# Kernel optimization log

Measured on AMD Instinct MI355X. Metric: run time of the kernel, lower is better.

## Reference

```python
import jax, jax.numpy as jnp
import numpy as np

B, T, M, F, N, H = 2, 1024, 1024, 1024, 16, 64
NEG = -1e30


def _relative_shift(x):
    # x: [b, n, q_len, k_len] -> Transformer-XL pad/reshape shift
    b, h, q_len, k_len = x.shape
    x = jnp.pad(x, ((0, 0), (0, 0), (0, 0), (1, 0)))
    x = x.reshape(b, h, k_len + 1, q_len)[:, :, 1:, :]
    return x.reshape(b, h, q_len, k_len)


def setup_inputs() -> dict:
    key = jax.random.key(0)
    ks = jax.random.split(key, 10)
    std = 0.02
    x = jax.random.normal(ks[0], (B, T, F), jnp.float32)
    rel = jax.random.normal(ks[1], (M + T, F), jnp.float32)
    memory = jax.random.normal(ks[2], (B, M, F), jnp.float32)
    episode_idx = jnp.sort(jax.random.randint(ks[3], (B, M), 0, 4), axis=-1).astype(jnp.int32)
    dones = jax.random.randint(ks[4], (B, T), 0, 2).astype(jnp.int32)
    Wq = jax.random.normal(ks[5], (F, N, H), jnp.float32) * std
    Wk = jax.random.normal(ks[6], (F, N, H), jnp.float32) * std
    Wv = jax.random.normal(ks[7], (F, N, H), jnp.float32) * std
    Wr = jax.random.normal(ks[8], (F, N, H), jnp.float32) * std
    u = jnp.zeros((N, H), jnp.float32)  # bias_init = zeros
    v = jnp.zeros((N, H), jnp.float32)
    Wout = jax.random.normal(ks[9], (N * H, F), jnp.float32) * std
    b_out = jnp.zeros((F,), jnp.float32)
    return {"x": x, "relative_positional_embeddings": rel, "memory": memory,
            "episode_idx": episode_idx, "dones": dones,
            "Wq": Wq, "Wk": Wk, "Wv": Wv, "Wr": Wr, "u": u, "v": v,
            "Wout": Wout, "b_out": b_out}


def reference(x, relative_positional_embeddings, memory, episode_idx, dones,
              Wq, Wk, Wv, Wr, u, v, Wout, b_out):
    scale = 1.0 / np.sqrt(H).astype(np.float32)
    # projections (no bias)
    q = jnp.einsum('btf,fnh->btnh', x, Wq)                      # [B,T,N,H]
    kv_in = jnp.concatenate([memory, x], axis=1)                # [B,M+T,F]
    k = jnp.einsum('bsf,fnh->bsnh', kv_in, Wk)                  # [B,M+T,N,H]
    val = jnp.einsum('bsf,fnh->bsnh', kv_in, Wv)                # [B,M+T,N,H]
    r = jnp.einsum('mf,fnh->mnh', relative_positional_embeddings, Wr)  # [M+T,N,H]

    q_u = q + u[None, None]
    q_v = q + v[None, None]

    # relative positional bias with TXL shift: [B,N,T,M+T]
    bd = jnp.einsum('btnh,mnh->bntm', q_v, r)
    bd = _relative_shift(bd)[..., -(M + T):]
    bias = bd * scale                                           # float32

    # episode mask + causal mask
    qi = episode_idx[:, -1:] + jnp.cumsum(dones, axis=1)        # [B,T]
    ki = jnp.concatenate([episode_idx, qi], axis=1)             # [B,M+T]
    ep_mask = qi[:, None, :, None] == ki[:, None, None, :]      # [B,1,T,M+T]
    causal = jnp.tril(jnp.ones((M + T, M + T), jnp.bool_))[-T:, :][None, None]
    mask = ep_mask & causal                                     # [B,1,T,M+T]

    # attention (matches jax.nn.dot_product_attention XLA path in bf16)
    logits = jnp.einsum('btnh,bsnh->bnts', q_u.astype(jnp.bfloat16), k.astype(jnp.bfloat16))
    logits = logits.astype(jnp.float32) * scale + bias          # [B,N,T,M+T]
    logits = jnp.where(mask, logits, NEG)
    probs = jax.nn.softmax(logits, axis=-1).astype(jnp.bfloat16)
    attn = jnp.einsum('bnts,bsnh->btnh', probs, val.astype(jnp.bfloat16))
    attn = attn.reshape(B, T, N * H).astype(jnp.float32)

    return attn @ Wout + b_out
```

## Files before the change

### kernel.cpp

```cpp
#include <hip/hip_runtime.h>
#include <cstdint>
#include <cstddef>

#define NB 2
#define TT 1024
#define MMEM 1024
#define SS 2048
#define FF 1024
#define NHD 16
#define HD 64

typedef __attribute__((ext_vector_type(8))) short bf16x8;
typedef __attribute__((ext_vector_type(4))) float f32x4;

__device__ __forceinline__ float bf2f(short s){
  unsigned u = ((unsigned)(unsigned short)s) << 16;
  float f; __builtin_memcpy(&f, &u, 4); return f;
}
__device__ __forceinline__ short f2bf(float f){
  unsigned u; __builtin_memcpy(&u, &f, 4);
  u += 0x7fffu + ((u >> 16) & 1u);
  return (short)(u >> 16);
}

typedef const __attribute__((address_space(1))) void gv_t;
typedef __attribute__((address_space(3))) void lv_t;
__device__ __forceinline__ void stage16(const void* g, void* l){
  __builtin_amdgcn_global_load_lds((gv_t*)g, (lv_t*)l, 16, 0, 0);
}

typedef __attribute__((address_space(3))) const short ls3_t;
__device__ __forceinline__ unsigned lds_off(const short* p){
  return (unsigned)(size_t)(ls3_t*)p;
}

template<int OFF>
__device__ __forceinline__ bf16x8 ds_read16(unsigned a){
  bf16x8 d;
  if constexpr (OFF == 0)
    asm volatile("ds_read_b128 %0, %1" : "=v"(d) : "v"(a));
  else
    asm volatile("ds_read_b128 %0, %1 offset:2048" : "=v"(d) : "v"(a));
  return d;
}


__global__ void build_inputs(const float* __restrict__ mem, const float* __restrict__ x,
                             const float* __restrict__ rel,
                             short* __restrict__ kv, short* __restrict__ relo){
  int i = blockIdx.x * blockDim.x + threadIdx.x;
  const int nkv = NB * SS * FF / 4;
  const float* src; short* dst;
  if (i < nkv){
    int idx = i * 4;
    int row = idx >> 10, col = idx & 1023;
    int b = row >> 11, s = row & 2047;
    src = (s < MMEM) ? (mem + ((size_t)b*MMEM + s)*FF + col)
                     : (x   + ((size_t)b*TT + (s - MMEM))*FF + col);
    dst = kv + (size_t)i * 4;
  } else {
    int j = i - nkv;
    if (j >= SS * FF / 4) return;
    src = rel + (size_t)j * 4;
    dst = relo + (size_t)j * 4;
  }
  float4 v = *(const float4*)src;
  short4 o; o.x = f2bf(v.x); o.y = f2bf(v.y); o.z = f2bf(v.z); o.w = f2bf(v.w);
  *(short4*)dst = o;
}

__global__ void transpose_cast5(const float* __restrict__ i0, const float* __restrict__ i1,
                                const float* __restrict__ i2, const float* __restrict__ i3,
                                const float* __restrict__ i4,
                                short* __restrict__ o0, short* __restrict__ o1,
                                short* __restrict__ o2, short* __restrict__ o3,
                                short* __restrict__ o4){
  const float* in; short* out;
  switch (blockIdx.z){
    case 0: in = i0; out = o0; break;
    case 1: in = i1; out = o1; break;
    case 2: in = i2; out = o2; break;
    case 3: in = i3; out = o3; break;
    default: in = i4; out = o4; break;
  }
  __shared__ float tile[32][33];
  int bx = blockIdx.x * 32, by = blockIdx.y * 32;
  int tx = threadIdx.x, ty = threadIdx.y;
  for (int j = ty; j < 32; j += 8)
    tile[j][tx] = in[(size_t)(by + j)*1024 + bx + tx];
  __syncthreads();
  for (int j = ty; j < 32; j += 8)
    out[(size_t)(bx + j)*1024 + by + tx] = f2bf(tile[tx][j]);
}

__global__ void scan_kernel(const int* __restrict__ episode_idx, const int* __restrict__ dones,
                            int* __restrict__ ki, int2* __restrict__ ranges){
  __shared__ int kis[SS];
  __shared__ int wsum[16];
  const int b = blockIdx.x, t = threadIdx.x;
  const int lane = t & 63, wv = t >> 6;
  int v = dones[b*TT + t];
  kis[t] = episode_idx[b*MMEM + t];
  #pragma unroll
  for (int off = 1; off < 64; off <<= 1){
    int tmp = __shfl_up(v, off, 64);
    if (lane >= off) v += tmp;
  }
  if (lane == 63) wsum[wv] = v;
  __syncthreads();
  int add = 0;
  for (int w = 0; w < wv; w++) add += wsum[w];
  v += add;
  const int base = kis[MMEM - 1];
  const int q = base + v;
  kis[MMEM + t] = q;
  ki[b*SS + t] = kis[t];
  ki[b*SS + MMEM + t] = q;
  __syncthreads();
  if (t < 64){
    const int qlo = kis[MMEM + t*16];
    const int qhi = kis[MMEM + t*16 + 15];
    int lo = 0, hi = SS;
    while (lo < hi){ int mid = (lo + hi) >> 1; if (kis[mid] < qlo) lo = mid + 1; else hi = mid; }
    const int s_lo = lo;
    lo = 0; hi = SS;
    const int tgt = qhi + 1;
    while (lo < hi){ int mid = (lo + hi) >> 1; if (kis[mid] < tgt) lo = mid + 1; else hi = mid; }
    int s_hi = lo;
    const int cap = t*16 + 15 + MMEM + 1;
    if (s_hi > cap) s_hi = cap;
    ranges[(b << 6) + t] = make_int2(s_lo, s_hi);
  }
}

__global__ void bias_tables(const short* __restrict__ kbf, const short* __restrict__ rbf,
                            const float* __restrict__ u, const float* __restrict__ v,
                            float* __restrict__ uk, float* __restrict__ vr){
  int i = blockIdx.x * blockDim.x + threadIdx.x;
  const short* p; const float* w; float* outp;
  if (i < NB * NHD * SS){
    int s = i & 2047, n = (i >> 11) & 15, b = i >> 15;
    p = kbf + (size_t)(b * SS + s) * 1024 + n * 64;
    w = u + n * 64;
    outp = uk + (size_t)(b * NHD + n) * SS + s;
  } else {
    int j = i - NB * NHD * SS;
    if (j >= NHD * SS) return;
    int jj = j & 2047, n = j >> 11;
    p = rbf + (size_t)jj * 1024 + n * 64;
    w = v + n * 64;
    outp = vr + (size_t)n * SS + jj;
  }
  float acc = 0.f;
  #pragma unroll
  for (int c = 0; c < 8; c++){
    bf16x8 kv8 = *(const bf16x8*)(p + c * 8);
    float4 w0 = *(const float4*)(w + c * 8);
    float4 w1 = *(const float4*)(w + c * 8 + 4);
    acc += bf2f(kv8[0])*w0.x + bf2f(kv8[1])*w0.y + bf2f(kv8[2])*w0.z + bf2f(kv8[3])*w0.w
         + bf2f(kv8[4])*w1.x + bf2f(kv8[5])*w1.y + bf2f(kv8[6])*w1.z + bf2f(kv8[7])*w1.w;
  }
  *outp = acc;
}

__device__ __forceinline__ void gemm_core_64x64(const short* __restrict__ A,
                                                const short* __restrict__ BT,
                                                int row0, int col0,
                                                short* As, short* Bs,
                                                f32x4 (&acc)[2][2]){
  const int tid = threadIdx.x;
  const int lane = tid & 63, wv = tid >> 6;
  const int lcol = lane & 15, quad = lane >> 4;
  const int wr = (wv >> 1) * 32, wc = (wv & 1) * 32;
  const int sw = lcol & 7;
  const int ch0 = (quad ^ sw) * 8;
  const int ch1 = ((4 + quad) ^ sw) * 8;

  #pragma unroll
  for (int r = 0; r < 2; r++)
    #pragma unroll
    for (int c = 0; c < 2; c++) acc[r][c] = (f32x4){0.f, 0.f, 0.f, 0.f};

  const int rs = tid >> 3, ps = tid & 7;
  const int ls = ps ^ (rs & 7);
  const short* gA = A  + (size_t)(row0 + rs) * 1024 + ls * 8;
  const short* gB = BT + (size_t)(col0 + rs) * 1024 + ls * 8;

  auto STAGE = [&](int k0, int bi){
    short* a = As + bi * 4096 + wv * 512;
    short* b = Bs + bi * 4096 + wv * 512;
    stage16(gA + k0,         a);
    stage16(gA + 32768 + k0, a + 2048);
    stage16(gB + k0,         b);
    stage16(gB + 32768 + k0, b + 2048);
  };

  const unsigned oa0 = lds_off(As) + (unsigned)(((wr + lcol) * 64 + ch0) * 2);
  const unsigned oa1 = lds_off(As) + (unsigned)(((wr + lcol) * 64 + ch1) * 2);
  const unsigned ob0 = lds_off(Bs) + (unsigned)(((wc + lcol) * 64 + ch0) * 2);
  const unsigned ob1 = lds_off(Bs) + (unsigned)(((wc + lcol) * 64 + ch1) * 2);

  STAGE(0, 0);
  STAGE(64, 1);

  #pragma unroll 1
  for (int i = 0; i < 16; ++i){
    const int cur = i - (i / 3) * 3;
    if (i <= 13){
      const int nb = (i + 2) - ((i + 2) / 3) * 3;
      STAGE((i + 2) << 6, nb);
      asm volatile("s_waitcnt vmcnt(8)" ::: "memory");
    } else if (i == 14){
      asm volatile("s_waitcnt vmcnt(4)" ::: "memory");
    } else {
      asm volatile("s_waitcnt vmcnt(0)" ::: "memory");
    }
    __builtin_amdgcn_s_barrier();
    __builtin_amdgcn_sched_barrier(0);
    const unsigned bo = (unsigned)(cur * 8192);
    bf16x8 b00 = ds_read16<0>(ob0 + bo);
    bf16x8 b01 = ds_read16<0>(ob1 + bo);
    bf16x8 b10 = ds_read16<2048>(ob0 + bo);
    bf16x8 b11 = ds_read16<2048>(ob1 + bo);
    bf16x8 a00 = ds_read16<0>(oa0 + bo);
    bf16x8 a01 = ds_read16<0>(oa1 + bo);
    bf16x8 a10 = ds_read16<2048>(oa0 + bo);
    bf16x8 a11 = ds_read16<2048>(oa1 + bo);
    asm volatile("s_waitcnt lgkmcnt(0)" ::: "memory");
    __builtin_amdgcn_sched_barrier(0);
    acc[0][0] = __builtin_amdgcn_mfma_f32_16x16x32_bf16(a00, b00, acc[0][0], 0, 0, 0);
    acc[0][0] = __builtin_amdgcn_mfma_f32_16x16x32_bf16(a01, b01, acc[0][0], 0, 0, 0);
    acc[0][1] = __builtin_amdgcn_mfma_f32_16x16x32_bf16(a00, b10, acc[0][1], 0, 0, 0);
    acc[0][1] = __builtin_amdgcn_mfma_f32_16x16x32_bf16(a01, b11, acc[0][1], 0, 0, 0);
    acc[1][0] = __builtin_amdgcn_mfma_f32_16x16x32_bf16(a10, b00, acc[1][0], 0, 0, 0);
    acc[1][0] = __builtin_amdgcn_mfma_f32_16x16x32_bf16(a11, b01, acc[1][0], 0, 0, 0);
    acc[1][1] = __builtin_amdgcn_mfma_f32_16x16x32_bf16(a10, b10, acc[1][1], 0, 0, 0);
    acc[1][1] = __builtin_amdgcn_mfma_f32_16x16x32_bf16(a11, b11, acc[1][1], 0, 0, 0);
    __builtin_amdgcn_sched_barrier(0);
    __builtin_amdgcn_s_barrier();
  }
}

__global__ __launch_bounds__(256) void proj_gemm(
    const short* __restrict__ kv, const short* __restrict__ relb,
    const short* __restrict__ WkT, const short* __restrict__ WvT,
    const short* __restrict__ WqT, const short* __restrict__ WrT,
    short* __restrict__ kbf, short* __restrict__ vT,
    short* __restrict__ qb, short* __restrict__ rbf,
    const int2* __restrict__ ranges){
  const int z = blockIdx.z;
  const int bx = blockIdx.x;
  const int tid = threadIdx.x;
  const short* A; const short* BT;
  int row0 = bx * 64, qbb = 0;
  __shared__ int s_jm;
  if (z == 0 || z == 1){
    const int bb = row0 >> 11;
    const int srow = row0 & 2047;
    if (srow + 64 <= ranges[bb << 6].x) return;
    A = kv; BT = (z == 0) ? WkT : WvT;
  }
  else if (z == 2){
    if (bx >= 32) return;
    qbb = bx >> 4;
    A = kv + (size_t)(qbb * SS + MMEM) * 1024;
    row0 = (bx & 15) * 64;
    BT = WqT;
  }
  else {
    if (bx >= 32) return;
    if (tid == 0) s_jm = 0x7fffffff;
    __syncthreads();
    if (tid < 128){
      int2 e = ranges[tid];
      int jr = (e.x & ~63) - ((tid & 63) << 4) + 1008;
      atomicMin(&s_jm, jr);
    }
    __syncthreads();
    if (row0 + 64 <= s_jm) return;
    A = relb; BT = WrT;
  }
  const int col0 = blockIdx.y * 64;

  __shared__ __align__(16) short As[3 * 64 * 64];
  __shared__ __align__(16) short Bs[3 * 64 * 64];
  f32x4 acc[2][2];
  gemm_core_64x64(A, BT, row0, col0, As, Bs, acc);

  const int lane = threadIdx.x & 63, wv = threadIdx.x >> 6;
  const int lcol = lane & 15, quad = lane >> 4;
  const int wr = (wv >> 1) * 32, wc = (wv & 1) * 32;
  #pragma unroll
  for (int c = 0; c < 2; c++){
    const int cc = col0 + wc + c*16 + lcol;
    #pragma unroll
    for (int r = 0; r < 2; r++){
      #pragma unroll
      for (int ri = 0; ri < 4; ri++){
        const int rr = row0 + wr + r*16 + quad*4 + ri;
        float val = acc[r][c][ri];
        if (z == 0){
          kbf[(size_t)rr * 1024 + cc] = f2bf(val);
        } else if (z == 1){
          int b = rr >> 11, s = rr & 2047;
          vT[(size_t)(((b << 4) + (cc >> 6)) * 64 + (cc & 63)) * 2048 + s] = f2bf(val);
        } else if (z == 2){
          qb[((size_t)(qbb * TT) + rr) * 1024 + cc] = f2bf(val);
        } else {
          rbf[(size_t)rr * 1024 + cc] = f2bf(val);
        }
      }
    }
  }
}

__global__ __launch_bounds__(256) void out_gemm(const short* __restrict__ A,
                                                const short* __restrict__ BT,
                                                const float* __restrict__ bias,
                                                float* __restrict__ C){
  const int row0 = blockIdx.x * 64, col0 = blockIdx.y * 64;
  __shared__ __align__(16) short As[3 * 64 * 64];
  __shared__ __align__(16) short Bs[3 * 64 * 64];
  f32x4 acc[2][2];
  gemm_core_64x64(A, BT, row0, col0, As, Bs, acc);

  const int lane = threadIdx.x & 63, wv = threadIdx.x >> 6;
  const int lcol = lane & 15, quad = lane >> 4;
  const int wr = (wv >> 1) * 32, wc = (wv & 1) * 32;
  #pragma unroll
  for (int c = 0; c < 2; c++){
    const int cc = col0 + wc + c*16 + lcol;
    const float bb = bias[cc];
    #pragma unroll
    for (int r = 0; r < 2; r++)
      #pragma unroll
      for (int ri = 0; ri < 4; ri++){
        const int rr = row0 + wr + r*16 + quad*4 + ri;
        C[(size_t)rr * 1024 + cc] = acc[r][c][ri] + bb;
      }
  }
}

__global__ __launch_bounds__(64) void attn_kernel(const short* __restrict__ qb,
                            const short* __restrict__ rbf,
                            const short* __restrict__ kk, const short* __restrict__ vT,
                            const int* __restrict__ ki,
                            const float* __restrict__ uk, const float* __restrict__ vr,
                            const int2* __restrict__ ranges,
                            short* __restrict__ attn_out){
  const int blk = blockIdx.x;
  const int xcd = blk & 7;
  const int idx = blk >> 3;
  const int bn  = (xcd << 2) | (idx >> 6);
  const int t16 = (idx & 63) * 16;
  const int n = bn & 15;
  const int b = bn >> 4;
  const int lane = threadIdx.x & 63;
  const int quad = lane >> 4, lcol = lane & 15;

  __shared__ __align__(16) short pb[16 * 72];

  const short* qp = qb + (size_t)(b * TT + t16 + lcol) * 1024 + n * 64 + quad * 8;
  bf16x8 aq0 = *(const bf16x8*)(qp);
  bf16x8 aq1 = *(const bf16x8*)(qp + 32);

  int trow[4], qi_r[4], sl[4];
  bool hi[4];
  #pragma unroll
  for (int r = 0; r < 4; r++){
    trow[r] = t16 + quad * 4 + r;
    qi_r[r] = ki[b * SS + MMEM + trow[r]];
    const int rt = quad * 4 + r;
    const int off = lcol + 15 - rt;
    sl[r] = quad * 16 + (off & 15);
    hi[r] = off >= 16;
  }

  float m_run[4], l_run[4];
  f32x4 o[4];
  #pragma unroll
  for (int r = 0; r < 4; r++){ m_run[r] = -1e30f; l_run[r] = 0.f; }
  #pragma unroll
  for (int c = 0; c < 4; c++) o[c] = (f32x4){0.f, 0.f, 0.f, 0.f};

  const float scale = 0.125f;
  const size_t vt_base = (size_t)((b * NHD + n) * HD);
  const short* rb_head = rbf + n * 64;
  const float* uk_row = uk + (size_t)(b * NHD + n) * SS;
  const float* vr_row = vr + (size_t)n * SS;

  const int2 rg = ranges[(b << 6) + (t16 >> 4)];
  const int kt0 = rg.x >> 6, kt1 = (rg.y - 1) >> 6;

  for (int kt = kt0; kt <= kt1; kt++){
    const int s0 = kt * 64;
    f32x4 sacc[4];
    float ukc[4];
    #pragma unroll
    for (int c = 0; c < 4; c++){
      const short* kp = kk + (size_t)(b * SS + s0 + 16 * c + lcol) * 1024 + n * 64 + quad * 8;
      bf16x8 b0 = *(const bf16x8*)(kp);
      bf16x8 b1 = *(const bf16x8*)(kp + 32);
      f32x4 z = (f32x4){0.f, 0.f, 0.f, 0.f};
      z = __builtin_amdgcn_mfma_f32_16x16x32_bf16(aq0, b0, z, 0, 0, 0);
      z = __builtin_amdgcn_mfma_f32_16x16x32_bf16(aq1, b1, z, 0, 0, 0);
      sacc[c] = z;
      ukc[c] = uk_row[s0 + 16 * c + lcol];
    }
    int ki_c[4];
    #pragma unroll
    for (int c = 0; c < 4; c++) ki_c[c] = ki[b * SS + s0 + 16 * c + lcol];

    const int j0 = s0 - t16 + 1008;
    f32x4 Dw[5];
    #pragma unroll
    for (int c5 = 0; c5 < 5; c5++){
      int jr = j0 + 16 * c5 + lcol;
      jr = (jr > SS - 1) ? (SS - 1) : jr;
      const short* rp = rb_head + (size_t)jr * 1024 + quad * 8;
      bf16x8 r0 = *(const bf16x8*)(rp);
      bf16x8 r1 = *(const bf16x8*)(rp + 32);
      f32x4 z = (f32x4){0.f, 0.f, 0.f, 0.f};
      z = __builtin_amdgcn_mfma_f32_16x16x32_bf16(aq0, r0, z, 0, 0, 0);
      z = __builtin_amdgcn_mfma_f32_16x16x32_bf16(aq1, r1, z, 0, 0, 0);
      const float vrj = vr_row[jr];
      #pragma unroll
      for (int r = 0; r < 4; r++) z[r] += vrj;
      Dw[c5] = z;
    }

    float p[4][4];
    float rowmax[4];
    #pragma unroll
    for (int r = 0; r < 4; r++) rowmax[r] = -1e30f;
    #pragma unroll
    for (int c = 0; c < 4; c++){
      const int s = s0 + 16 * c + lcol;
      #pragma unroll
      for (int r = 0; r < 4; r++){
        const float v0 = __shfl(Dw[c][r], sl[r], 64);
        const float v1 = __shfl(Dw[c + 1][r], sl[r], 64);
        const float bd = hi[r] ? v1 : v0;
        float lg = (sacc[c][r] + ukc[c] + bd) * scale;
        const bool valid = (s <= trow[r] + MMEM) && (ki_c[c] == qi_r[r]);
        lg = valid ? lg : -1e30f;
        p[c][r] = lg;
        rowmax[r] = fmaxf(rowmax[r], lg);
      }
    }
    #pragma unroll
    for (int r = 0; r < 4; r++){
      float vmx = rowmax[r];
      #pragma unroll
      for (int off = 1; off < 16; off <<= 1) vmx = fmaxf(vmx, __shfl_xor(vmx, off, 64));
      float mnew = fmaxf(m_run[r], vmx);
      float alpha = __expf(m_run[r] - mnew);
      m_run[r] = mnew;
      l_run[r] *= alpha;
      #pragma unroll
      for (int c = 0; c < 4; c++) o[c][r] *= alpha;
    }
    float psum[4] = {0.f, 0.f, 0.f, 0.f};
    #pragma unroll
    for (int c = 0; c < 4; c++)
      #pragma unroll
      for (int r = 0; r < 4; r++){
        float pv = __expf(p[c][r] - m_run[r]);
        p[c][r] = pv;
        psum[r] += pv;
      }
    #pragma unroll
    for (int r = 0; r < 4; r++){
      float vs = psum[r];
      #pragma unroll
      for (int off = 1; off < 16; off <<= 1) vs += __shfl_xor(vs, off, 64);
      l_run[r] += vs;
    }
    #pragma unroll
    for (int c = 0; c < 4; c++)
      #pragma unroll
      for (int r = 0; r < 4; r++)
        pb[(quad * 4 + r) * 72 + 16 * c + lcol] = f2bf(p[c][r]);
    bf16x8 pa0 = *(const bf16x8*)(&pb[lcol * 72 + quad * 8]);
    bf16x8 pa1 = *(const bf16x8*)(&pb[lcol * 72 + 32 + quad * 8]);
    #pragma unroll
    for (int c = 0; c < 4; c++){
      const short* vtp = vT + (vt_base + c * 16 + lcol) * (size_t)SS + s0 + quad * 8;
      bf16x8 bv0 = *(const bf16x8*)(vtp);
      bf16x8 bv1 = *(const bf16x8*)(vtp + 32);
      o[c] = __builtin_amdgcn_mfma_f32_16x16x32_bf16(pa0, bv0, o[c], 0, 0, 0);
      o[c] = __builtin_amdgcn_mfma_f32_16x16x32_bf16(pa1, bv1, o[c], 0, 0, 0);
    }
  }

  #pragma unroll
  for (int r = 0; r < 4; r++){
    const float inv = 1.f / l_run[r];
    const int t = trow[r];
    #pragma unroll
    for (int c = 0; c < 4; c++)
      attn_out[(size_t)(b * TT + t) * 1024 + n * 64 + c * 16 + lcol] = f2bf(o[c][r] * inv);
  }
}

extern "C" void kernel_launch(void* const* d_in, const int* in_sizes, int n_in,
                              void* d_out, int out_size, void* d_ws, size_t ws_size,
                              hipStream_t stream){
  const float* x      = (const float*)d_in[0];
  const float* rel    = (const float*)d_in[1];
  const float* memory = (const float*)d_in[2];
  const int*   episode_idx = (const int*)d_in[3];
  const int*   dones  = (const int*)d_in[4];
  const float* Wq  = (const float*)d_in[5];
  const float* Wk  = (const float*)d_in[6];
  const float* Wv  = (const float*)d_in[7];
  const float* Wr  = (const float*)d_in[8];
  const float* u   = (const float*)d_in[9];
  const float* v   = (const float*)d_in[10];
  const float* Wout  = (const float*)d_in[11];
  const float* b_out = (const float*)d_in[12];
  float* out = (float*)d_out;

  char* ws = (char*)d_ws;
  size_t off = 0;
  auto alloc = [&](size_t bytes) -> char* {
    char* p = ws + off;
    off += (bytes + 255) & ~(size_t)255;
    return p;
  };
  short* kv_bf  = (short*)alloc((size_t)NB * SS * FF * 2);
  short* rel_bf = (short*)alloc((size_t)SS * FF * 2);
  short* WqT    = (short*)alloc((size_t)FF * 1024 * 2);
  short* WkT    = (short*)alloc((size_t)FF * 1024 * 2);
  short* WvT    = (short*)alloc((size_t)FF * 1024 * 2);
  short* WrT    = (short*)alloc((size_t)FF * 1024 * 2);
  short* WoT    = (short*)alloc((size_t)FF * 1024 * 2);
  short* qbuf   = (short*)alloc((size_t)NB * TT * 1024 * 2);
  short* kbf    = (short*)alloc((size_t)NB * SS * 1024 * 2);
  short* vTb    = (short*)alloc((size_t)NB * SS * 1024 * 2);
  short* rbf    = (short*)alloc((size_t)SS * 1024 * 2);
  int*   ki     = (int*)  alloc((size_t)NB * SS * 4);
  int2*  ranges = (int2*) alloc((size_t)NB * 64 * 8);
  float* ukT    = (float*)alloc((size_t)NB * NHD * SS * 4);
  float* vrT    = (float*)alloc((size_t)NHD * SS * 4);
  short* attn   = (short*)alloc((size_t)NB * TT * 1024 * 2);
  (void)ws_size; (void)in_sizes; (void)n_in; (void)out_size;

  const int n4 = NB*SS*FF/4 + SS*FF/4;
  build_inputs<<<(n4 + 255)/256, 256, 0, stream>>>(memory, x, rel, kv_bf, rel_bf);
  dim3 tb(32, 8), tg5(32, 32, 5);
  transpose_cast5<<<tg5, tb, 0, stream>>>(Wq, Wk, Wv, Wr, Wout, WqT, WkT, WvT, WrT, WoT);
  scan_kernel<<<NB, TT, 0, stream>>>(episode_idx, dones, ki, ranges);

  proj_gemm<<<dim3(64, 16, 4), 256, 0, stream>>>(kv_bf, rel_bf,
                                                 WkT, WvT, WqT, WrT,
                                                 kbf, vTb, qbuf, rbf, ranges);

  bias_tables<<<(NB*NHD*SS + NHD*SS + 255)/256, 256, 0, stream>>>(kbf, rbf, u, v, ukT, vrT);

  attn_kernel<<<2048, 64, 0, stream>>>(qbuf, rbf, kbf, vTb, ki, ukT, vrT, ranges, attn);

  out_gemm<<<dim3(32, 16), 256, 0, stream>>>(attn, WoT, b_out, out);
}
```

Before: 217.3 us.

## Fuse prep kernels into one launch and XCD-swizzle GEMM block mapping

Merges the input cast, weight transpose-cast and episode scan into one kernel whose block index picks the sub-task, so two launches are removed. The scan now uses 256 threads, each handling 4 elements. The proj and out GEMMs flatten their grids and remap block IDs so that blocks sharing the same A rows land on the same XCD, aiming at better L2 reuse. The risks are a heavier prep kernel that needs more shared memory per block and swizzle arithmetic that assumes a fixed grid shape.

```diff
diff --git a/kernel.cpp b/kernel.cpp
--- a/kernel.cpp
+++ b/kernel.cpp
@@ -44,92 +44,115 @@
   return d;
 }
 
-
-__global__ void build_inputs(const float* __restrict__ mem, const float* __restrict__ x,
-                             const float* __restrict__ rel,
-                             short* __restrict__ kv, short* __restrict__ relo){
-  int i = blockIdx.x * blockDim.x + threadIdx.x;
-  const int nkv = NB * SS * FF / 4;
-  const float* src; short* dst;
-  if (i < nkv){
-    int idx = i * 4;
-    int row = idx >> 10, col = idx & 1023;
-    int b = row >> 11, s = row & 2047;
-    src = (s < MMEM) ? (mem + ((size_t)b*MMEM + s)*FF + col)
-                     : (x   + ((size_t)b*TT + (s - MMEM))*FF + col);
-    dst = kv + (size_t)i * 4;
-  } else {
-    int j = i - nkv;
-    if (j >= SS * FF / 4) return;
-    src = rel + (size_t)j * 4;
-    dst = relo + (size_t)j * 4;
-  }
-  float4 v = *(const float4*)src;
-  short4 o; o.x = f2bf(v.x); o.y = f2bf(v.y); o.z = f2bf(v.z); o.w = f2bf(v.w);
-  *(short4*)dst = o;
-}
-
-__global__ void transpose_cast5(const float* __restrict__ i0, const float* __restrict__ i1,
-                                const float* __restrict__ i2, const float* __restrict__ i3,
-                                const float* __restrict__ i4,
-                                short* __restrict__ o0, short* __restrict__ o1,
-                                short* __restrict__ o2, short* __restrict__ o3,
-                                short* __restrict__ o4){
-  const float* in; short* out;
-  switch (blockIdx.z){
-    case 0: in = i0; out = o0; break;
-    case 1: in = i1; out = o1; break;
-    case 2: in = i2; out = o2; break;
-    case 3: in = i3; out = o3; break;
-    default: in = i4; out = o4; break;
-  }
-  __shared__ float tile[32][33];
-  int bx = blockIdx.x * 32, by = blockIdx.y * 32;
-  int tx = threadIdx.x, ty = threadIdx.y;
-  for (int j = ty; j < 32; j += 8)
-    tile[j][tx] = in[(size_t)(by + j)*1024 + bx + tx];
-  __syncthreads();
-  for (int j = ty; j < 32; j += 8)
-    out[(size_t)(bx + j)*1024 + by + tx] = f2bf(tile[tx][j]);
-}
-
-__global__ void scan_kernel(const int* __restrict__ episode_idx, const int* __restrict__ dones,
-                            int* __restrict__ ki, int2* __restrict__ ranges){
-  __shared__ int kis[SS];
-  __shared__ int wsum[16];
-  const int b = blockIdx.x, t = threadIdx.x;
-  const int lane = t & 63, wv = t >> 6;
-  int v = dones[b*TT + t];
-  kis[t] = episode_idx[b*MMEM + t];
-  #pragma unroll
-  for (int off = 1; off < 64; off <<= 1){
-    int tmp = __shfl_up(v, off, 64);
-    if (lane >= off) v += tmp;
-  }
-  if (lane == 63) wsum[wv] = v;
-  __syncthreads();
-  int add = 0;
-  for (int w = 0; w < wv; w++) add += wsum[w];
-  v += add;
-  const int base = kis[MMEM - 1];
-  const int q = base + v;
-  kis[MMEM + t] = q;
-  ki[b*SS + t] = kis[t];
-  ki[b*SS + MMEM + t] = q;
-  __syncthreads();
-  if (t < 64){
-    const int qlo = kis[MMEM + t*16];
-    const int qhi = kis[MMEM + t*16 + 15];
-    int lo = 0, hi = SS;
-    while (lo < hi){ int mid = (lo + hi) >> 1; if (kis[mid] < qlo) lo = mid + 1; else hi = mid; }
-    const int s_lo = lo;
-    lo = 0; hi = SS;
-    const int tgt = qhi + 1;
-    while (lo < hi){ int mid = (lo + hi) >> 1; if (kis[mid] < tgt) lo = mid + 1; else hi = mid; }
-    int s_hi = lo;
-    const int cap = t*16 + 15 + MMEM + 1;
-    if (s_hi > cap) s_hi = cap;
-    ranges[(b << 6) + t] = make_int2(s_lo, s_hi);
+#define NKVB 6144
+#define NTRB 5120
+
+__global__ __launch_bounds__(256) void prep_kernel(
+    const float* __restrict__ mem, const float* __restrict__ x,
+    const float* __restrict__ rel,
+    const int* __restrict__ episode_idx, const int* __restrict__ dones,
+    const float* __restrict__ w0, const float* __restrict__ w1,
+    const float* __restrict__ w2, const float* __restrict__ w3,
+    const float* __restrict__ w4,
+    short* __restrict__ kv, short* __restrict__ relo,
+    short* __restrict__ o0, short* __restrict__ o1,
+    short* __restrict__ o2, short* __restrict__ o3, short* __restrict__ o4,
+    int* __restrict__ ki, int2* __restrict__ ranges){
+  const int blk = blockIdx.x;
+  const int tid = threadIdx.x;
+
+  if (blk < NKVB){
+    int i = blk * 256 + tid;
+    const int nkv = NB * SS * FF / 4;
+    const float* src; short* dst;
+    if (i < nkv){
+      int idx = i * 4;
+      int row = idx >> 10, col = idx & 1023;
+      int b = row >> 11, s = row & 2047;
+      src = (s < MMEM) ? (mem + ((size_t)b*MMEM + s)*FF + col)
+                       : (x   + ((size_t)b*TT + (s - MMEM))*FF + col);
+      dst = kv + (size_t)i * 4;
+    } else {
+      int j = i - nkv;
+      src = rel + (size_t)j * 4;
+      dst = relo + (size_t)j * 4;
+    }
+    float4 v = *(const float4*)src;
+    short4 o; o.x = f2bf(v.x); o.y = f2bf(v.y); o.z = f2bf(v.z); o.w = f2bf(v.w);
+    *(short4*)dst = o;
+    return;
+  }
+
+  if (blk < NKVB + NTRB){
+    const int j = blk - NKVB;
+    const int z5 = j >> 10;
+    const int rem = j & 1023;
+    const int by5 = rem >> 5, bx5 = rem & 31;
+    const float* in; short* out;
+    switch (z5){
+      case 0: in = w0; out = o0; break;
+      case 1: in = w1; out = o1; break;
+      case 2: in = w2; out = o2; break;
+      case 3: in = w3; out = o3; break;
+      default: in = w4; out = o4; break;
+    }
+    __shared__ float tile[32][33];
+    const int bx = bx5 * 32, by = by5 * 32;
+    const int tx = tid & 31, ty = tid >> 5;
+    for (int jj = ty; jj < 32; jj += 8)
+      tile[jj][tx] = in[(size_t)(by + jj)*1024 + bx + tx];
+    __syncthreads();
+    for (int jj = ty; jj < 32; jj += 8)
+      out[(size_t)(bx + jj)*1024 + by + tx] = f2bf(tile[tx][jj]);
+    return;
+  }
+
+  {
+    const int b = blk - (NKVB + NTRB);
+    __shared__ int kis[SS];
+    __shared__ int wsum[4];
+    const int t = tid;
+    const int lane = t & 63, wv = t >> 6;
+    #pragma unroll
+    for (int j = 0; j < 4; j++) kis[t*4 + j] = episode_idx[b*MMEM + t*4 + j];
+    int d[4]; int s = 0;
+    #pragma unroll
+    for (int j = 0; j < 4; j++){ d[j] = dones[b*TT + t*4 + j]; s += d[j]; }
+    int v = s;
+    #pragma unroll
+    for (int off = 1; off < 64; off <<= 1){
+      int tmp = __shfl_up(v, off, 64);
+      if (lane >= off) v += tmp;
+    }
+    if (lane == 63) wsum[wv] = v;
+    __syncthreads();
+    int add = 0;
+    for (int w = 0; w < wv; w++) add += wsum[w];
+    const int base = kis[MMEM - 1];
+    int run = add + v - s;
+    #pragma unroll
+    for (int j = 0; j < 4; j++){
+      run += d[j];
+      const int q = base + run;
+      kis[MMEM + t*4 + j] = q;
+      ki[b*SS + MMEM + t*4 + j] = q;
+      ki[b*SS + t*4 + j] = kis[t*4 + j];
+    }
+    __syncthreads();
+    if (t < 64){
+      const int qlo = kis[MMEM + t*16];
+      const int qhi = kis[MMEM + t*16 + 15];
+      int lo = 0, hi = SS;
+      while (lo < hi){ int mid = (lo + hi) >> 1; if (kis[mid] < qlo) lo = mid + 1; else hi = mid; }
+      const int s_lo = lo;
+      lo = 0; hi = SS;
+      const int tgt = qhi + 1;
+      while (lo < hi){ int mid = (lo + hi) >> 1; if (kis[mid] < tgt) lo = mid + 1; else hi = mid; }
+      int s_hi = lo;
+      const int cap = t*16 + 15 + MMEM + 1;
+      if (s_hi > cap) s_hi = cap;
+      ranges[(b << 6) + t] = make_int2(s_lo, s_hi);
+    }
   }
 }
 
@@ -249,7 +272,10 @@
     short* __restrict__ qb, short* __restrict__ rbf,
     const int2* __restrict__ ranges){
   const int z = blockIdx.z;
-  const int bx = blockIdx.x;
+  const int iswz = blockIdx.x;
+  const int xcd = iswz & 7, jj = iswz >> 3;
+  const int bx = ((jj >> 4) << 3) | xcd;
+  const int col0 = (jj & 15) * 64;
   const int tid = threadIdx.x;
   const short* A; const short* BT;
   int row0 = bx * 64, qbb = 0;
@@ -280,7 +306,6 @@
     if (row0 + 64 <= s_jm) return;
     A = relb; BT = WrT;
   }
-  const int col0 = blockIdx.y * 64;
 
   __shared__ __align__(16) short As[3 * 64 * 64];
   __shared__ __align__(16) short Bs[3 * 64 * 64];
@@ -318,7 +343,10 @@
                                                 const short* __restrict__ BT,
                                                 const float* __restrict__ bias,
                                                 float* __restrict__ C){
-  const int row0 = blockIdx.x * 64, col0 = blockIdx.y * 64;
+  const int iswz = blockIdx.x;
+  const int xcd = iswz & 7, jj = iswz >> 3;
+  const int p = ((jj >> 4) << 3) | xcd;
+  const int row0 = p * 64, col0 = (jj & 15) * 64;
   __shared__ __align__(16) short As[3 * 64 * 64];
   __shared__ __align__(16) short Bs[3 * 64 * 64];
   f32x4 acc[2][2];
@@ -546,19 +574,18 @@
   short* attn   = (short*)alloc((size_t)NB * TT * 1024 * 2);
   (void)ws_size; (void)in_sizes; (void)n_in; (void)out_size;
 
-  const int n4 = NB*SS*FF/4 + SS*FF/4;
-  build_inputs<<<(n4 + 255)/256, 256, 0, stream>>>(memory, x, rel, kv_bf, rel_bf);
-  dim3 tb(32, 8), tg5(32, 32, 5);
-  transpose_cast5<<<tg5, tb, 0, stream>>>(Wq, Wk, Wv, Wr, Wout, WqT, WkT, WvT, WrT, WoT);
-  scan_kernel<<<NB, TT, 0, stream>>>(episode_idx, dones, ki, ranges);
-
-  proj_gemm<<<dim3(64, 16, 4), 256, 0, stream>>>(kv_bf, rel_bf,
-                                                 WkT, WvT, WqT, WrT,
-                                                 kbf, vTb, qbuf, rbf, ranges);
+  prep_kernel<<<NKVB + NTRB + NB, 256, 0, stream>>>(
+      memory, x, rel, episode_idx, dones,
+      Wq, Wk, Wv, Wr, Wout,
+      kv_bf, rel_bf, WqT, WkT, WvT, WrT, WoT, ki, ranges);
+
+  proj_gemm<<<dim3(1024, 1, 4), 256, 0, stream>>>(kv_bf, rel_bf,
+                                                  WkT, WvT, WqT, WrT,
+                                                  kbf, vTb, qbuf, rbf, ranges);
 
   bias_tables<<<(NB*NHD*SS + NHD*SS + 255)/256, 256, 0, stream>>>(kbf, rbf, u, v, ukT, vrT);
 
   attn_kernel<<<2048, 64, 0, stream>>>(qbuf, rbf, kbf, vTb, ki, ukT, vrT, ranges, attn);
 
-  out_gemm<<<dim3(32, 16), 256, 0, stream>>>(attn, WoT, b_out, out);
-}
+  out_gemm<<<512, 256, 0, stream>>>(attn, WoT, b_out, out);
+}
```

New measurement: 202.2 us. 6.9% less time.
